# Optimization experiments

Measured on AMD Instinct MI355X. Metric: run time of the kernel, lower is better.

## Reference

```python
import jax, jax.numpy as jnp
import numpy as np

N_NODES = 50000
N_EDGES = 800000
HIDDEN = 128
EDGE_DIM = 16
N_HEADS = 8
HEAD_DIM = HIDDEN // N_HEADS
SCALE = 1.0 / np.sqrt(HEAD_DIM).astype(np.float32)
LN_EPS = 1e-5


def setup_inputs() -> dict:
    key = jax.random.key(0)
    ks = jax.random.split(key, 24)
    s = 0.02

    def w(k, shape):
        return jax.random.normal(k, shape, dtype=jnp.float32) * s

    inp = {
        "node_features": jax.random.normal(ks[0], (N_NODES, HIDDEN), dtype=jnp.float32),
        "edge_index": jax.random.randint(ks[1], (2, N_EDGES), 0, N_NODES, dtype=jnp.int32),
        "edge_features": jax.random.normal(ks[2], (N_EDGES, EDGE_DIM), dtype=jnp.float32),
        # projections stored as [in, out] (y = x @ W + b)
        "Wq": w(ks[3], (HIDDEN, HIDDEN)), "bq": jnp.zeros((HIDDEN,), jnp.float32),
        "Wk": w(ks[4], (HIDDEN, HIDDEN)), "bk": jnp.zeros((HIDDEN,), jnp.float32),
        "Wv": w(ks[5], (HIDDEN, HIDDEN)), "bv": jnp.zeros((HIDDEN,), jnp.float32),
        "Wb1": w(ks[6], (EDGE_DIM, N_HEADS)), "bb1": jnp.zeros((N_HEADS,), jnp.float32),
        "Wb2": w(ks[7], (N_HEADS, N_HEADS)), "bb2": jnp.zeros((N_HEADS,), jnp.float32),
        "Wo": w(ks[8], (HIDDEN, HIDDEN)), "bo": jnp.zeros((HIDDEN,), jnp.float32),
        "Wf1": w(ks[9], (HIDDEN, 2 * HIDDEN)), "bf1": jnp.zeros((2 * HIDDEN,), jnp.float32),
        "Wf2": w(ks[10], (2 * HIDDEN, HIDDEN)), "bf2": jnp.zeros((HIDDEN,), jnp.float32),
        "g1": jnp.ones((HIDDEN,), jnp.float32), "be1": jnp.zeros((HIDDEN,), jnp.float32),
        "g2": jnp.ones((HIDDEN,), jnp.float32), "be2": jnp.zeros((HIDDEN,), jnp.float32),
    }
    return inp


def _layer_norm(x, gamma, beta):
    mu = jnp.mean(x, axis=-1, keepdims=True)
    var = jnp.mean(jnp.square(x - mu), axis=-1, keepdims=True)
    return (x - mu) * jax.lax.rsqrt(var + LN_EPS) * gamma + beta


def reference(node_features, edge_index, edge_features,
              Wq, bq, Wk, bk, Wv, bv, Wb1, bb1, Wb2, bb2,
              Wo, bo, Wf1, bf1, Wf2, bf2, g1, be1, g2, be2):
    n_nodes = node_features.shape[0]
    src, dst = edge_index[0], edge_index[1]

    q = (node_features @ Wq + bq).reshape(n_nodes, N_HEADS, HEAD_DIM)
    k = (node_features @ Wk + bk).reshape(n_nodes, N_HEADS, HEAD_DIM)
    v = (node_features @ Wv + bv).reshape(n_nodes, N_HEADS, HEAD_DIM)

    # per-edge attention logits [E, H]
    edge_bias = jax.nn.silu(edge_features @ Wb1 + bb1) @ Wb2 + bb2
    logits = jnp.sum(q[dst] * k[src], axis=-1) * SCALE + edge_bias

    # segment softmax over edges sharing the same dst node
    max_s = jax.ops.segment_max(logits, dst, num_segments=n_nodes)
    exp_s = jnp.exp(logits - max_s[dst])
    norm = jax.ops.segment_sum(exp_s, dst, num_segments=n_nodes)
    attn = exp_s / jnp.clip(norm[dst], 1e-12)

    # weighted aggregation [N, H, D] -> [N, hidden]
    weighted = attn[:, :, None] * v[src]
    aggregated = jax.ops.segment_sum(weighted, dst, num_segments=n_nodes)
    aggregated = aggregated.reshape(n_nodes, HIDDEN)

    x = _layer_norm(node_features + (aggregated @ Wo + bo), g1, be1)
    ffn = jax.nn.silu(x @ Wf1 + bf1) @ Wf2 + bf2
    return _layer_norm(x + ffn, g2, be2)
```

## Files before the change

### kernel.cpp

```cpp
#include <hip/hip_runtime.h>
#include <hip/hip_bf16.h>
#include <math.h>

#define HIDDEN 128
#define EDGE_DIM 16
#define N_HEADS 8
#define QK_SCALE 0.25f
#define LN_EPS 1e-5f
#define EB_SCALE 256.0f
#define EB_INV (1.0f / 256.0f)

using bf16x8 = __attribute__((ext_vector_type(8))) short;
using f32x4 = __attribute__((ext_vector_type(4))) float;
using f32x4v = __attribute__((ext_vector_type(4))) float;
using f32x2 = __attribute__((ext_vector_type(2))) float;
using i32x4 = __attribute__((ext_vector_type(4))) int;
typedef __hip_bfloat16 bf16;

__device__ __forceinline__ float b2f(short u) {
  union { unsigned int i; float f; } c;
  c.i = ((unsigned int)(unsigned short)u) << 16;
  return c.f;
}
__device__ __forceinline__ short f2b(float f) {
  bf16 h = __float2bfloat16(f);
  union { bf16 b; short s; } c;
  c.b = h;
  return c.s;
}
__device__ __forceinline__ unsigned char f2fp8(float f) {
  int pk = __builtin_amdgcn_cvt_pk_fp8_f32(f, f, 0, false);
  return (unsigned char)(pk & 0xff);
}

__global__ __launch_bounds__(256) void conv_weights_kernel(
    const float* __restrict__ Wq, const float* __restrict__ Wk, const float* __restrict__ Wv,
    const float* __restrict__ bq, const float* __restrict__ bk, const float* __restrict__ bv,
    const float* __restrict__ Wo, const float* __restrict__ Wf1, const float* __restrict__ Wf2,
    bf16* __restrict__ Wqkv_t, bf16* __restrict__ Wo_t, bf16* __restrict__ Wf1_t,
    bf16* __restrict__ Wf2_t, float* __restrict__ bqkv) {
  int i = blockIdx.x * 256 + threadIdx.x;
  if (i < 49152) {
    int n = i >> 7, k = i & 127;
    const float* W = (n < 128) ? Wq : ((n < 256) ? Wk : Wv);
    int nn = n & 127;
    Wqkv_t[i] = __float2bfloat16(W[k * 128 + nn]);
  } else if (i < 65536) {
    int j = i - 49152;
    int n = j >> 7, k = j & 127;
    Wo_t[j] = __float2bfloat16(Wo[k * 128 + n]);
  } else if (i < 98304) {
    int j = i - 65536;
    int n = j >> 7, k = j & 127;
    Wf1_t[j] = __float2bfloat16(Wf1[k * 256 + n]);
  } else if (i < 131072) {
    int j = i - 98304;
    int n = j >> 8, k = j & 255;
    Wf2_t[j] = __float2bfloat16(Wf2[k * 128 + n]);
  }
  if (i < 384) bqkv[i] = (i < 128) ? bq[i] : ((i < 256) ? bk[i - 128] : bv[i - 256]);
}

template <int K, int EPI, int OUTBF, int AF32>
__global__ __launch_bounds__(256) void mfma_gemm_kernel(
    const void* __restrict__ Ap, const bf16* __restrict__ Wt,
    const float* __restrict__ bias, void* __restrict__ Cout, int M, int Nc) {
  const int tid = threadIdx.x;
  const int w = tid >> 6, l = tid & 63;
  const int wr = w >> 1, wc = w & 1;
  const int lr = l & 15, lk = l >> 4;
  const int bm = blockIdx.y * 64;
  const int bn = blockIdx.x * 128 + wc * 64;

  f32x4 acc[2][4] = {};
  const int arow0 = bm + wr * 32 + lr;

  for (int k0 = 0; k0 < K; k0 += 128) {
    bf16x8 bfr[4][4];
#pragma unroll
    for (int fn = 0; fn < 4; ++fn) {
      const bf16* wp = Wt + (size_t)(bn + fn * 16 + lr) * K + k0 + lk * 8;
#pragma unroll
      for (int ks = 0; ks < 4; ++ks) bfr[fn][ks] = *(const bf16x8*)(wp + ks * 32);
    }
    bf16x8 afr[2][4];
#pragma unroll
    for (int fr = 0; fr < 2; ++fr) {
      int row = arow0 + fr * 16;
      if (row >= M) row = M - 1;
      if (AF32) {
        const float* ap = (const float*)Ap + (size_t)row * K + k0 + lk * 8;
#pragma unroll
        for (int ks = 0; ks < 4; ++ks) {
          float4 x = *(const float4*)(ap + ks * 32);
          float4 y = *(const float4*)(ap + ks * 32 + 4);
          bf16x8 t;
          t[0] = f2b(x.x); t[1] = f2b(x.y); t[2] = f2b(x.z); t[3] = f2b(x.w);
          t[4] = f2b(y.x); t[5] = f2b(y.y); t[6] = f2b(y.z); t[7] = f2b(y.w);
          afr[fr][ks] = t;
        }
      } else {
        const bf16* ap = (const bf16*)Ap + (size_t)row * K + k0 + lk * 8;
#pragma unroll
        for (int ks = 0; ks < 4; ++ks) afr[fr][ks] = *(const bf16x8*)(ap + ks * 32);
      }
    }
#pragma unroll
    for (int ks = 0; ks < 4; ++ks)
#pragma unroll
      for (int fr = 0; fr < 2; ++fr)
#pragma unroll
        for (int fn = 0; fn < 4; ++fn)
          acc[fr][fn] = __builtin_amdgcn_mfma_f32_16x16x32_bf16(afr[fr][ks], bfr[fn][ks],
                                                                acc[fr][fn], 0, 0, 0);
  }

#pragma unroll
  for (int fn = 0; fn < 4; ++fn) {
    const int col = bn + fn * 16 + lr;
    const float bv = bias[col];
#pragma unroll
    for (int fr = 0; fr < 2; ++fr) {
      const int rbase = bm + wr * 32 + fr * 16 + lk * 4;
#pragma unroll
      for (int r = 0; r < 4; ++r) {
        int row = rbase + r;
        if (row < M) {
          float o = acc[fr][fn][r] + bv;
          if (EPI == 1) o = o / (1.f + __expf(-o));
          if (OUTBF)
            ((bf16*)Cout)[(size_t)row * Nc + col] = __float2bfloat16(o);
          else
            ((float*)Cout)[(size_t)row * Nc + col] = o;
        }
      }
    }
  }
}

__global__ __launch_bounds__(256) void mfma_gemm_qkv_kernel(
    const float* __restrict__ A, const bf16* __restrict__ Wt,
    const float* __restrict__ bias, bf16* __restrict__ qb,
    unsigned char* __restrict__ kv8, int M) {
  __shared__ __align__(16) char lds[64 * 272];
  const int tid = threadIdx.x;
  const int w = tid >> 6, l = tid & 63;
  const int wr = w >> 1, wc = w & 1;
  const int lr = l & 15, lk = l >> 4;
  const int bm = blockIdx.x * 64;
  const int arow0 = bm + wr * 32 + lr;

  bf16x8 afr[2][4];
#pragma unroll
  for (int fr = 0; fr < 2; ++fr) {
    int row = arow0 + fr * 16;
    if (row >= M) row = M - 1;
    const float* ap = A + (size_t)row * 128 + lk * 8;
#pragma unroll
    for (int ks = 0; ks < 4; ++ks) {
      float4 x = *(const float4*)(ap + ks * 32);
      float4 y = *(const float4*)(ap + ks * 32 + 4);
      bf16x8 t;
      t[0] = f2b(x.x); t[1] = f2b(x.y); t[2] = f2b(x.z); t[3] = f2b(x.w);
      t[4] = f2b(y.x); t[5] = f2b(y.y); t[6] = f2b(y.z); t[7] = f2b(y.w);
      afr[fr][ks] = t;
    }
  }

  const int row2 = tid >> 2, seg = tid & 3;
  const int grow = bm + row2;

#pragma unroll
  for (int s = 0; s < 3; ++s) {
    const int bn = s * 128 + wc * 64;
    bf16x8 bfr[4][4];
#pragma unroll
    for (int fn = 0; fn < 4; ++fn) {
      const bf16* wp = Wt + (size_t)(bn + fn * 16 + lr) * 128 + lk * 8;
#pragma unroll
      for (int ks = 0; ks < 4; ++ks) bfr[fn][ks] = *(const bf16x8*)(wp + ks * 32);
    }
    f32x4 acc[2][4] = {};
#pragma unroll
    for (int ks = 0; ks < 4; ++ks)
#pragma unroll
      for (int fr = 0; fr < 2; ++fr)
#pragma unroll
        for (int fn = 0; fn < 4; ++fn)
          acc[fr][fn] = __builtin_amdgcn_mfma_f32_16x16x32_bf16(afr[fr][ks], bfr[fn][ks],
                                                                acc[fr][fn], 0, 0, 0);

    if (s > 0) __syncthreads();
    if (s == 0) {
      short* sq = (short*)lds;
#pragma unroll
      for (int fn = 0; fn < 4; ++fn) {
        const int col = wc * 64 + fn * 16 + lr;
        const float bv = bias[bn + fn * 16 + lr];
#pragma unroll
        for (int fr = 0; fr < 2; ++fr) {
#pragma unroll
          for (int r = 0; r < 4; ++r) {
            int rl = wr * 32 + fr * 16 + lk * 4 + r;
            sq[rl * 136 + col] = f2b(acc[fr][fn][r] + bv);
          }
        }
      }
    } else {
      unsigned char* s8 = (unsigned char*)lds;
#pragma unroll
      for (int fn = 0; fn < 4; ++fn) {
        const int col = wc * 64 + fn * 16 + lr;
        const float bv = bias[bn + fn * 16 + lr];
#pragma unroll
        for (int fr = 0; fr < 2; ++fr) {
#pragma unroll
          for (int r = 0; r < 4; ++r) {
            int rl = wr * 32 + fr * 16 + lk * 4 + r;
            s8[rl * 144 + col] = f2fp8(acc[fr][fn][r] + bv);
          }
        }
      }
    }
    __syncthreads();

    if (grow < M) {
      if (s == 0) {
        const int4* src = (const int4*)(lds + row2 * 272 + seg * 64);
        int4* dst = (int4*)(qb + (size_t)grow * 128 + seg * 32);
        dst[0] = src[0];
        dst[1] = src[1];
        dst[2] = src[2];
        dst[3] = src[3];
      } else {
        const int4* src = (const int4*)(lds + row2 * 144 + seg * 32);
        int4* dst = (int4*)(kv8 + (size_t)grow * 256 + (s == 1 ? 0 : 128) + seg * 32);
        dst[0] = src[0];
        dst[1] = src[1];
      }
    }
  }
}

template <int K>
__global__ __launch_bounds__(256) void mfma_gemm_ln_kernel(
    const bf16* __restrict__ A, const bf16* __restrict__ Wt,
    const float* __restrict__ bias, const float* __restrict__ R,
    const float* __restrict__ gam, const float* __restrict__ bet,
    float* __restrict__ y, bf16* __restrict__ yb, int M) {
  const int tid = threadIdx.x;
  const int w = tid >> 6, l = tid & 63;
  const int wr = w >> 1, wc = w & 1;
  const int lr = l & 15, lk = l >> 4;
  const int bm = blockIdx.x * 64;
  const int bn = wc * 64;

  f32x4 acc[2][4] = {};
  const int arow0 = bm + wr * 32 + lr;

  for (int k0 = 0; k0 < K; k0 += 128) {
    bf16x8 bfr[4][4];
#pragma unroll
    for (int fn = 0; fn < 4; ++fn) {
      const bf16* wp = Wt + (size_t)(bn + fn * 16 + lr) * K + k0 + lk * 8;
#pragma unroll
      for (int ks = 0; ks < 4; ++ks) bfr[fn][ks] = *(const bf16x8*)(wp + ks * 32);
    }
    bf16x8 afr[2][4];
#pragma unroll
    for (int fr = 0; fr < 2; ++fr) {
      int row = arow0 + fr * 16;
      if (row >= M) row = M - 1;
      const bf16* ap = A + (size_t)row * K + k0 + lk * 8;
#pragma unroll
      for (int ks = 0; ks < 4; ++ks) afr[fr][ks] = *(const bf16x8*)(ap + ks * 32);
    }
#pragma unroll
    for (int ks = 0; ks < 4; ++ks)
#pragma unroll
      for (int fr = 0; fr < 2; ++fr)
#pragma unroll
        for (int fn = 0; fn < 4; ++fn)
          acc[fr][fn] = __builtin_amdgcn_mfma_f32_16x16x32_bf16(afr[fr][ks], bfr[fn][ks],
                                                                acc[fr][fn], 0, 0, 0);
  }

  float bv[4], gv[4], ev[4];
#pragma unroll
  for (int fn = 0; fn < 4; ++fn) {
    int col = bn + fn * 16 + lr;
    bv[fn] = bias[col];
    gv[fn] = gam[col];
    ev[fn] = bet[col];
  }
  float ps[2][4], psq[2][4];
#pragma unroll
  for (int fr = 0; fr < 2; ++fr) {
#pragma unroll
    for (int r = 0; r < 4; ++r) {
      int row = bm + wr * 32 + fr * 16 + lk * 4 + r;
      int rrow = (row < M) ? row : (M - 1);
      float s = 0.f, sq = 0.f;
#pragma unroll
      for (int fn = 0; fn < 4; ++fn) {
        int col = bn + fn * 16 + lr;
        float o = acc[fr][fn][r] + bv[fn] + R[(size_t)rrow * HIDDEN + col];
        acc[fr][fn][r] = o;
        s += o;
        sq += o * o;
      }
      ps[fr][r] = s;
      psq[fr][r] = sq;
    }
  }
#pragma unroll
  for (int off = 1; off < 16; off <<= 1) {
#pragma unroll
    for (int fr = 0; fr < 2; ++fr)
#pragma unroll
      for (int r = 0; r < 4; ++r) {
        ps[fr][r] += __shfl_xor(ps[fr][r], off, 64);
        psq[fr][r] += __shfl_xor(psq[fr][r], off, 64);
      }
  }
  __shared__ float s_sum[2][64], s_sq[2][64];
  if (lr == 0) {
#pragma unroll
    for (int fr = 0; fr < 2; ++fr)
#pragma unroll
      for (int r = 0; r < 4; ++r) {
        int rl = wr * 32 + fr * 16 + lk * 4 + r;
        s_sum[wc][rl] = ps[fr][r];
        s_sq[wc][rl] = psq[fr][r];
      }
  }
  __syncthreads();
#pragma unroll
  for (int fr = 0; fr < 2; ++fr) {
#pragma unroll
    for (int r = 0; r < 4; ++r) {
      int rl = wr * 32 + fr * 16 + lk * 4 + r;
      int row = bm + rl;
      float tot = s_sum[0][rl] + s_sum[1][rl];
      float tsq = s_sq[0][rl] + s_sq[1][rl];
      float mean = tot * (1.f / 128.f);
      float var = tsq * (1.f / 128.f) - mean * mean;
      float rstd = rsqrtf(var + LN_EPS);
      if (row < M) {
#pragma unroll
        for (int fn = 0; fn < 4; ++fn) {
          int col = bn + fn * 16 + lr;
          float val = (acc[fr][fn][r] - mean) * rstd * gv[fn] + ev[fn];
          if (y) y[(size_t)row * HIDDEN + col] = val;
          if (yb) yb[(size_t)row * HIDDEN + col] = __float2bfloat16(val);
        }
      }
    }
  }
}

__global__ void hist_kernel(const int* __restrict__ dst, int* __restrict__ counts, int E) {
  int e = blockIdx.x * blockDim.x + threadIdx.x;
  if (e < E) atomicAdd(&counts[dst[e]], 1);
}

__device__ __forceinline__ int wave_incl_scan(int x, int lane) {
  int incl = x;
#pragma unroll
  for (int off = 1; off < 64; off <<= 1) {
    int y = __shfl_up(incl, off, 64);
    if (lane >= off) incl += y;
  }
  return incl;
}

__global__ __launch_bounds__(256) void scan_block_kernel(const int* __restrict__ counts,
                                                         int* __restrict__ offs,
                                                         int* __restrict__ btot, int N) {
  __shared__ int s4[4];
  int tid = threadIdx.x;
  int i = blockIdx.x * 256 + tid;
  int lane = tid & 63, wv = tid >> 6;
  int x = (i < N) ? counts[i] : 0;
  int incl = wave_incl_scan(x, lane);
  if (lane == 63) s4[wv] = incl;
  __syncthreads();
  if (tid == 0) {
    int s = 0;
#pragma unroll
    for (int j = 0; j < 4; ++j) { int t = s4[j]; s4[j] = s; s += t; }
    btot[blockIdx.x] = s;
  }
  __syncthreads();
  if (i < N) offs[i] = s4[wv] + incl - x;
}

__global__ __launch_bounds__(256) void scan_tot_kernel(int* __restrict__ btot, int nb) {
  __shared__ int s4[4];
  __shared__ int carry;
  int tid = threadIdx.x;
  int lane = tid & 63, wv = tid >> 6;
  if (tid == 0) carry = 0;
  __syncthreads();
  for (int c0 = 0; c0 < nb; c0 += 256) {
    int i = c0 + tid;
    int x = (i < nb) ? btot[i] : 0;
    int incl = wave_incl_scan(x, lane);
    if (lane == 63) s4[wv] = incl;
    __syncthreads();
    if (tid == 0) {
      int s = 0;
#pragma unroll
      for (int j = 0; j < 4; ++j) { int t = s4[j]; s4[j] = s; s += t; }
    }
    __syncthreads();
    int base = carry + s4[wv];
    if (i < nb) btot[i] = base + incl - x;
    __syncthreads();
    if (tid == 255) carry = base + incl;
    __syncthreads();
  }
}

__global__ __launch_bounds__(256) void scan_add_kernel(int* __restrict__ offs,
                                                       const int* __restrict__ btot,
                                                       int N, int E) {
  int i = blockIdx.x * 256 + threadIdx.x;
  if (i < N) offs[i] += btot[blockIdx.x];
  if (i == 0) offs[N] = E;
}

__global__ __launch_bounds__(256) void scatter_mlp_kernel(
    const int* __restrict__ dst, const int* __restrict__ src,
    const float* __restrict__ ef, const float* __restrict__ Wb1,
    const float* __restrict__ bb1, const float* __restrict__ Wb2,
    const float* __restrict__ bb2, const int* __restrict__ offs,
    int* __restrict__ cursor, i32x4* __restrict__ es16, int E) {
  __shared__ float w1[128], w2[64], b1[8], b2[8];
  int tid = threadIdx.x;
  if (tid < 128) w1[tid] = Wb1[tid];
  else if (tid < 192) w2[tid - 128] = Wb2[tid - 128];
  else if (tid < 200) b1[tid - 192] = bb1[tid - 192];
  else if (tid < 208) b2[tid - 200] = bb2[tid - 200];
  __syncthreads();

  int e = blockIdx.x * 256 + tid;
  if (e >= E) return;

  const f32x4v* p4 = (const f32x4v*)(ef + (size_t)e * 16);
  f32x4v f0 = __builtin_nontemporal_load(p4 + 0);
  f32x4v f1 = __builtin_nontemporal_load(p4 + 1);
  f32x4v f2 = __builtin_nontemporal_load(p4 + 2);
  f32x4v f3 = __builtin_nontemporal_load(p4 + 3);
  float x[16] = {f0[0], f0[1], f0[2], f0[3], f1[0], f1[1], f1[2], f1[3],
                 f2[0], f2[1], f2[2], f2[3], f3[0], f3[1], f3[2], f3[3]};

  float h[8];
#pragma unroll
  for (int j = 0; j < 8; ++j) h[j] = b1[j];
#pragma unroll
  for (int i = 0; i < 16; ++i) {
    float xi = x[i];
#pragma unroll
    for (int j = 0; j < 8; ++j) h[j] = fmaf(xi, w1[i * 8 + j], h[j]);
  }
#pragma unroll
  for (int j = 0; j < 8; ++j) h[j] = h[j] / (1.f + __expf(-h[j]));

  float o[8];
#pragma unroll
  for (int j = 0; j < 8; ++j) o[j] = b2[j];
#pragma unroll
  for (int jj = 0; jj < 8; ++jj) {
    float hj = h[jj];
#pragma unroll
    for (int j = 0; j < 8; ++j) o[j] = fmaf(hj, w2[jj * 8 + j], o[j]);
  }

  int lo = __builtin_amdgcn_cvt_pk_fp8_f32(o[0] * EB_SCALE, o[1] * EB_SCALE, 0, false);
  lo = __builtin_amdgcn_cvt_pk_fp8_f32(o[2] * EB_SCALE, o[3] * EB_SCALE, lo, true);
  int hi = __builtin_amdgcn_cvt_pk_fp8_f32(o[4] * EB_SCALE, o[5] * EB_SCALE, 0, false);
  hi = __builtin_amdgcn_cvt_pk_fp8_f32(o[6] * EB_SCALE, o[7] * EB_SCALE, hi, true);

  int d = dst[e];
  int p = offs[d] + atomicAdd(&cursor[d], 1);
  i32x4 rec;
  rec[0] = src[e]; rec[1] = lo; rec[2] = hi; rec[3] = 0;
  es16[p] = rec;
}

__global__ __launch_bounds__(256) void node_attn_kernel(
    const bf16* __restrict__ qb, const unsigned char* __restrict__ kv8,
    const i32x4* __restrict__ es16, const int* __restrict__ offs,
    bf16* __restrict__ agg, int Nn) {
  int n = blockIdx.x * 4 + (threadIdx.x >> 6);
  if (n >= Nn) return;
  int l = threadIdx.x & 63;
  int g = l >> 3;
  int il = l & 7;

  int s0 = offs[n], s1 = offs[n + 1];
  bf16* orow = agg + (size_t)n * HIDDEN + il * 16;
  if (s0 >= s1) {
    if (g == 0) {
      bf16x8 z = {};
      *(bf16x8*)(orow) = z;
      *(bf16x8*)(orow + 8) = z;
    }
    return;
  }

  const bf16* qrow = qb + (size_t)n * 128 + il * 16;
  bf16x8 qa = *(const bf16x8*)(qrow);
  bf16x8 qb8 = *(const bf16x8*)(qrow + 8);
  float qf[16];
#pragma unroll
  for (int j = 0; j < 8; ++j) {
    qf[j] = b2f(qa[j]) * QK_SCALE;
    qf[8 + j] = b2f(qb8[j]) * QK_SCALE;
  }

  float lsum = 0.f;
  float acc[16] = {};
  const int ebshift = (il & 2) << 3;

  for (int p0 = s0; p0 < s1; p0 += 8) {
    int p = p0 + g;
    bool valid = p < s1;
    int pc = valid ? p : s1 - 1;
    i32x4 rec = es16[pc];
    int cs = rec[0];
    unsigned ebw = (unsigned)((il < 4) ? rec[1] : rec[2]);
    f32x2 ebp = __builtin_amdgcn_cvt_pk_f32_fp8(ebw >> ebshift, false);
    float ebv = ((il & 1) ? ebp[1] : ebp[0]) * EB_INV;

    const unsigned char* kvrow = kv8 + (size_t)cs * 256 + il * 16;
    i32x4 kw = *(const i32x4*)(kvrow);
    i32x4 vw = *(const i32x4*)(kvrow + 128);

    float prod = 0.f;
#pragma unroll
    for (int w2 = 0; w2 < 4; ++w2) {
      f32x2 lo = __builtin_amdgcn_cvt_pk_f32_fp8(kw[w2], false);
      f32x2 hi = __builtin_amdgcn_cvt_pk_f32_fp8(kw[w2], true);
      prod = fmaf(qf[w2 * 4 + 0], lo[0], prod);
      prod = fmaf(qf[w2 * 4 + 1], lo[1], prod);
      prod = fmaf(qf[w2 * 4 + 2], hi[0], prod);
      prod = fmaf(qf[w2 * 4 + 3], hi[1], prod);
    }
    float pe = valid ? __expf(prod + ebv) : 0.f;
    lsum += pe;
#pragma unroll
    for (int w2 = 0; w2 < 4; ++w2) {
      f32x2 lo = __builtin_amdgcn_cvt_pk_f32_fp8(vw[w2], false);
      f32x2 hi = __builtin_amdgcn_cvt_pk_f32_fp8(vw[w2], true);
      acc[w2 * 4 + 0] = fmaf(pe, lo[0], acc[w2 * 4 + 0]);
      acc[w2 * 4 + 1] = fmaf(pe, lo[1], acc[w2 * 4 + 1]);
      acc[w2 * 4 + 2] = fmaf(pe, hi[0], acc[w2 * 4 + 2]);
      acc[w2 * 4 + 3] = fmaf(pe, hi[1], acc[w2 * 4 + 3]);
    }
  }

#pragma unroll
  for (int off = 8; off < 64; off <<= 1) {
    lsum += __shfl_xor(lsum, off, 64);
#pragma unroll
    for (int j = 0; j < 16; ++j) acc[j] += __shfl_xor(acc[j], off, 64);
  }

  if (g == 0) {
    float inv = (lsum > 0.f) ? 1.f / lsum : 0.f;
    bf16x8 o0, o1;
#pragma unroll
    for (int j = 0; j < 8; ++j) {
      o0[j] = f2b(acc[j] * inv);
      o1[j] = f2b(acc[8 + j] * inv);
    }
    *(bf16x8*)(orow) = o0;
    *(bf16x8*)(orow + 8) = o1;
  }
}

extern "C" void kernel_launch(void* const* d_in, const int* in_sizes, int n_in,
                              void* d_out, int out_size, void* d_ws, size_t ws_size,
                              hipStream_t stream) {
  const float* nf = (const float*)d_in[0];
  const int* ei = (const int*)d_in[1];
  const float* ef = (const float*)d_in[2];
  const float* Wq = (const float*)d_in[3];
  const float* bq = (const float*)d_in[4];
  const float* Wk = (const float*)d_in[5];
  const float* bk_ = (const float*)d_in[6];
  const float* Wv = (const float*)d_in[7];
  const float* bv = (const float*)d_in[8];
  const float* Wb1 = (const float*)d_in[9];
  const float* bb1 = (const float*)d_in[10];
  const float* Wb2 = (const float*)d_in[11];
  const float* bb2 = (const float*)d_in[12];
  const float* Wo = (const float*)d_in[13];
  const float* bo = (const float*)d_in[14];
  const float* Wf1 = (const float*)d_in[15];
  const float* bf1 = (const float*)d_in[16];
  const float* Wf2 = (const float*)d_in[17];
  const float* bf2 = (const float*)d_in[18];
  const float* g1 = (const float*)d_in[19];
  const float* be1 = (const float*)d_in[20];
  const float* g2 = (const float*)d_in[21];
  const float* be2 = (const float*)d_in[22];

  const int N = in_sizes[0] / HIDDEN;
  const int E = in_sizes[2] / EDGE_DIM;
  const int* srcA = ei;
  const int* dstA = ei + E;

  char* base = (char*)d_ws;
  size_t off = 0;
  auto alloc = [&](size_t bytes) {
    off = (off + 255) & ~(size_t)255;
    char* p = base + off;
    off += bytes;
    return p;
  };

  size_t qb_bytes = (size_t)N * 128 * 2;
  size_t kv_bytes = (size_t)N * 256;
  size_t hb_bytes = (size_t)N * 256 * 2;
  char* regB = alloc(hb_bytes > qb_bytes + kv_bytes ? hb_bytes : qb_bytes + kv_bytes);
  bf16* qb = (bf16*)regB;
  unsigned char* kv8 = (unsigned char*)(regB + qb_bytes);
  bf16* hbuf = (bf16*)regB;
  bf16* agg = (bf16*)alloc((size_t)N * HIDDEN * 2);
  float* x1 = (float*)alloc((size_t)N * HIDDEN * 4);
  bf16* x1b = (bf16*)alloc((size_t)N * HIDDEN * 2);
  i32x4* es16 = (i32x4*)alloc((size_t)E * 16);
  int* counts = (int*)alloc((size_t)N * 8);
  int* cursor = counts + N;
  int* offs = (int*)alloc((size_t)(N + 1) * 4);
  const int nb = (N + 255) / 256;
  int* btot = (int*)alloc((size_t)nb * 4);
  bf16* Wqkv_t = (bf16*)alloc(384 * 128 * 2);
  bf16* Wo_t = (bf16*)alloc(128 * 128 * 2);
  bf16* Wf1_t = (bf16*)alloc(256 * 128 * 2);
  bf16* Wf2_t = (bf16*)alloc(128 * 256 * 2);
  float* bqkv = (float*)alloc(384 * 4);

  float* outp = (float*)d_out;
  const int mb64 = (N + 63) / 64;
  const int eblocks = (E + 255) / 256;

  conv_weights_kernel<<<512, 256, 0, stream>>>(Wq, Wk, Wv, bq, bk_, bv, Wo, Wf1, Wf2,
                                               Wqkv_t, Wo_t, Wf1_t, Wf2_t, bqkv);

  mfma_gemm_qkv_kernel<<<mb64, 256, 0, stream>>>(nf, Wqkv_t, bqkv, qb, kv8, N);

  hipMemsetAsync(counts, 0, (size_t)N * 8, stream);
  hist_kernel<<<eblocks, 256, 0, stream>>>(dstA, counts, E);
  scan_block_kernel<<<nb, 256, 0, stream>>>(counts, offs, btot, N);
  scan_tot_kernel<<<1, 256, 0, stream>>>(btot, nb);
  scan_add_kernel<<<nb, 256, 0, stream>>>(offs, btot, N, E);
  scatter_mlp_kernel<<<eblocks, 256, 0, stream>>>(dstA, srcA, ef, Wb1, bb1, Wb2, bb2,
                                                  offs, cursor, es16, E);

  node_attn_kernel<<<(N + 3) / 4, 256, 0, stream>>>(qb, kv8, es16, offs, agg, N);

  mfma_gemm_ln_kernel<128><<<mb64, 256, 0, stream>>>(agg, Wo_t, bo, nf, g1, be1, x1, x1b, N);

  mfma_gemm_kernel<128, 1, 1, 0><<<dim3(2, mb64), 256, 0, stream>>>(
      x1b, Wf1_t, bf1, hbuf, N, 256);

  mfma_gemm_ln_kernel<256><<<mb64, 256, 0, stream>>>(hbuf, Wf2_t, bf2, x1, g2, be2,
                                                     outp, nullptr, N);
}
```

Baseline: 265.9 us.

## Split edge MLP from CSR scatter and gather edge records via index

```diff
diff --git a/kernel.cpp b/kernel.cpp
--- a/kernel.cpp
+++ b/kernel.cpp
@@ -430,12 +430,11 @@
   if (i == 0) offs[N] = E;
 }
 
-__global__ __launch_bounds__(256) void scatter_mlp_kernel(
-    const int* __restrict__ dst, const int* __restrict__ src,
-    const float* __restrict__ ef, const float* __restrict__ Wb1,
-    const float* __restrict__ bb1, const float* __restrict__ Wb2,
-    const float* __restrict__ bb2, const int* __restrict__ offs,
-    int* __restrict__ cursor, i32x4* __restrict__ es16, int E) {
+__global__ __launch_bounds__(256) void mlp_seq_kernel(
+    const int* __restrict__ src, const float* __restrict__ ef,
+    const float* __restrict__ Wb1, const float* __restrict__ bb1,
+    const float* __restrict__ Wb2, const float* __restrict__ bb2,
+    i32x4* __restrict__ es_seq, int E) {
   __shared__ float w1[128], w2[64], b1[8], b2[8];
   int tid = threadIdx.x;
   if (tid < 128) w1[tid] = Wb1[tid];
@@ -482,17 +481,25 @@
   int hi = __builtin_amdgcn_cvt_pk_fp8_f32(o[4] * EB_SCALE, o[5] * EB_SCALE, 0, false);
   hi = __builtin_amdgcn_cvt_pk_fp8_f32(o[6] * EB_SCALE, o[7] * EB_SCALE, hi, true);
 
+  i32x4 rec;
+  rec[0] = src[e]; rec[1] = lo; rec[2] = hi; rec[3] = 0;
+  __builtin_nontemporal_store(rec, es_seq + e);
+}
+
+__global__ __launch_bounds__(256) void place_kernel(
+    const int* __restrict__ dst, const int* __restrict__ offs,
+    int* __restrict__ cursor, int* __restrict__ eid_csr, int E) {
+  int e = blockIdx.x * 256 + threadIdx.x;
+  if (e >= E) return;
   int d = dst[e];
   int p = offs[d] + atomicAdd(&cursor[d], 1);
-  i32x4 rec;
-  rec[0] = src[e]; rec[1] = lo; rec[2] = hi; rec[3] = 0;
-  es16[p] = rec;
+  eid_csr[p] = e;
 }
 
 __global__ __launch_bounds__(256) void node_attn_kernel(
     const bf16* __restrict__ qb, const unsigned char* __restrict__ kv8,
-    const i32x4* __restrict__ es16, const int* __restrict__ offs,
-    bf16* __restrict__ agg, int Nn) {
+    const i32x4* __restrict__ es_seq, const int* __restrict__ eid_csr,
+    const int* __restrict__ offs, bf16* __restrict__ agg, int Nn) {
   int n = blockIdx.x * 4 + (threadIdx.x >> 6);
   if (n >= Nn) return;
   int l = threadIdx.x & 63;
@@ -524,13 +531,17 @@
   float acc[16] = {};
   const int ebshift = (il & 2) << 3;
 
+  int pc0 = (s0 + g < s1) ? (s0 + g) : (s1 - 1);
+  i32x4 rec = es_seq[eid_csr[pc0]];
+
   for (int p0 = s0; p0 < s1; p0 += 8) {
-    int p = p0 + g;
-    bool valid = p < s1;
-    int pc = valid ? p : s1 - 1;
-    i32x4 rec = es16[pc];
-    int cs = rec[0];
-    unsigned ebw = (unsigned)((il < 4) ? rec[1] : rec[2]);
+    bool valid = (p0 + g) < s1;
+    i32x4 cur = rec;
+    int pn = p0 + 8 + g;
+    if (pn < s1) rec = es_seq[eid_csr[pn]];
+
+    int cs = cur[0];
+    unsigned ebw = (unsigned)((il < 4) ? cur[1] : cur[2]);
     f32x2 ebp = __builtin_amdgcn_cvt_pk_f32_fp8(ebw >> ebshift, false);
     float ebv = ((il & 1) ? ebp[1] : ebp[0]) * EB_INV;
 
@@ -632,7 +643,8 @@
   bf16* agg = (bf16*)alloc((size_t)N * HIDDEN * 2);
   float* x1 = (float*)alloc((size_t)N * HIDDEN * 4);
   bf16* x1b = (bf16*)alloc((size_t)N * HIDDEN * 2);
-  i32x4* es16 = (i32x4*)alloc((size_t)E * 16);
+  i32x4* es_seq = (i32x4*)alloc((size_t)E * 16);
+  int* eid_csr = (int*)alloc((size_t)E * 4);
   int* counts = (int*)alloc((size_t)N * 8);
   int* cursor = counts + N;
   int* offs = (int*)alloc((size_t)(N + 1) * 4);
@@ -653,15 +665,17 @@
 
   mfma_gemm_qkv_kernel<<<mb64, 256, 0, stream>>>(nf, Wqkv_t, bqkv, qb, kv8, N);
 
+  mlp_seq_kernel<<<eblocks, 256, 0, stream>>>(srcA, ef, Wb1, bb1, Wb2, bb2, es_seq, E);
+
   hipMemsetAsync(counts, 0, (size_t)N * 8, stream);
   hist_kernel<<<eblocks, 256, 0, stream>>>(dstA, counts, E);
   scan_block_kernel<<<nb, 256, 0, stream>>>(counts, offs, btot, N);
   scan_tot_kernel<<<1, 256, 0, stream>>>(btot, nb);
   scan_add_kernel<<<nb, 256, 0, stream>>>(offs, btot, N, E);
-  scatter_mlp_kernel<<<eblocks, 256, 0, stream>>>(dstA, srcA, ef, Wb1, bb1, Wb2, bb2,
-                                                  offs, cursor, es16, E);
-
-  node_attn_kernel<<<(N + 3) / 4, 256, 0, stream>>>(qb, kv8, es16, offs, agg, N);
+  place_kernel<<<eblocks, 256, 0, stream>>>(dstA, offs, cursor, eid_csr, E);
+
+  node_attn_kernel<<<(N + 3) / 4, 256, 0, stream>>>(qb, kv8, es_seq, eid_csr, offs,
+                                                    agg, N);
 
   mfma_gemm_ln_kernel<128><<<mb64, 256, 0, stream>>>(agg, Wo_t, bo, nf, g1, be1, x1, x1b, N);
 
```

Result: slower. 284.1 us (+6.8%).
